# Optimization experiments

Hardware: AMD Instinct MI355X
Metric: run time of the kernel (lower is better)

## Reference

```python
import jax, jax.numpy as jnp
import numpy as np

B, N = 128, 196
ENC, DEC, ATT = 2048, 512, 512

def setup_inputs() -> dict:
    key = jax.random.key(0)
    ks = jax.random.split(key, 8)
    s_enc = 1.0 / np.sqrt(ENC)
    s_dec = 1.0 / np.sqrt(DEC)
    s_att = 1.0 / np.sqrt(ATT)
    return {
        "encoder_out": jax.random.normal(ks[0], (B, N, ENC), jnp.float32),
        "decoder_hidden": jax.random.normal(ks[1], (B, DEC), jnp.float32),
        "W_enc": jax.random.uniform(ks[2], (ENC, ATT), jnp.float32, -s_enc, s_enc),
        "b_enc": jax.random.uniform(ks[3], (ATT,), jnp.float32, -s_enc, s_enc),
        "W_dec": jax.random.uniform(ks[4], (DEC, ATT), jnp.float32, -s_dec, s_dec),
        "b_dec": jax.random.uniform(ks[5], (ATT,), jnp.float32, -s_dec, s_dec),
        "W_full": jax.random.uniform(ks[6], (ATT,), jnp.float32, -s_att, s_att),
        "b_full": jax.random.uniform(ks[7], (), jnp.float32, -s_att, s_att),
    }

def reference(encoder_out, decoder_hidden, W_enc, b_enc, W_dec, b_dec, W_full, b_full):
    # att1: [B, N, ATT]; att2: [B, 1, ATT]
    att1 = jnp.einsum('bne,ea->bna', encoder_out, W_enc) + b_enc
    att2 = decoder_hidden @ W_dec + b_dec
    combined = jax.nn.relu(att1 + att2[:, None, :])
    e = jnp.einsum('bna,a->bn', combined, W_full) + b_full  # [B, N]
    alpha = jax.nn.softmax(e, axis=1)
    attention_weighted_encoding = jnp.einsum('bne,bn->be', encoder_out, alpha)
    return attention_weighted_encoding, alpha
```

## Files before the change

kernel.cpp:

```cpp
#include <hip/hip_runtime.h>
#include <hip/hip_bf16.h>

#define BB   128
#define NN   196
#define MM   (BB*NN)
#define ENC  2048
#define ATT  512
#define DEC  512
#define BK   32
#define KSTEPS (ENC/BK)

using f32x4 = __attribute__((ext_vector_type(4))) float;
using s16x8 = __attribute__((ext_vector_type(8))) short;

__device__ __forceinline__ short f2bf(float f) {
    union { __hip_bfloat16 h; short s; } u;
    u.h = __float2bfloat16(f);
    return u.s;
}

__global__ void transpose_convert_kernel(const float* __restrict__ W,
                                         unsigned short* __restrict__ Wt) {
    __shared__ float tile[32][33];
    const int a0 = blockIdx.x * 32;
    const int k0 = blockIdx.y * 32;
    const int tx = threadIdx.x & 31, ty = threadIdx.x >> 5;
    #pragma unroll
    for (int i = 0; i < 32; i += 8)
        tile[ty + i][tx] = W[(size_t)(k0 + ty + i) * ATT + a0 + tx];
    __syncthreads();
    #pragma unroll
    for (int i = 0; i < 32; i += 8) {
        union { __hip_bfloat16 h; unsigned short u; } v;
        v.h = __float2bfloat16(tile[tx][ty + i]);
        Wt[(size_t)(a0 + ty + i) * ENC + k0 + tx] = v.u;
    }
}

__global__ void att2_kernel(const float* __restrict__ dec,
                            const float* __restrict__ Wd,
                            const float* __restrict__ bd,
                            const float* __restrict__ benc,
                            float* __restrict__ att2) {
    const int b  = blockIdx.x;
    const int c0 = blockIdx.y * 64;
    const int t  = threadIdx.x;
    const int cl = t & 63, kg = t >> 6;
    __shared__ float sdec[DEC];
    __shared__ float red[4][64];
    sdec[t]       = dec[b * DEC + t];
    sdec[t + 256] = dec[b * DEC + t + 256];
    __syncthreads();
    float acc = 0.f;
    const float* wp = Wd + c0 + cl;
    #pragma unroll 8
    for (int k = kg * 128; k < kg * 128 + 128; ++k)
        acc += sdec[k] * wp[(size_t)k * ATT];
    red[kg][cl] = acc;
    __syncthreads();
    if (t < 64) {
        float s = red[0][t] + red[1][t] + red[2][t] + red[3][t];
        att2[b * ATT + c0 + t] = s + bd[c0 + t] + benc[c0 + t];
    }
}

__global__ __launch_bounds__(256, 5)
void gemm_e_kernel(const float* __restrict__ enc,
                   const unsigned short* __restrict__ Wt,
                   const float* __restrict__ att2,
                   const float* __restrict__ Wf,
                   float* __restrict__ e_part) {
    __shared__ float sA[64 * 32];
    __shared__ unsigned short sB[128 * 32];
    __shared__ float e_sm[64];

    const int t    = threadIdx.x;
    const int lane = t & 63;
    const int w    = t >> 6;
    const int aBlk  = blockIdx.x;
    const int mBase = blockIdx.y * 64;
    const int aBase = aBlk * 128;
    const int r = lane & 15, q = lane >> 4;

    const float* gA[2];
    #pragma unroll
    for (int i = 0; i < 2; ++i) {
        int s = i * 256 + t;
        int row = s >> 3, ck = s & 7;
        int g = ck ^ (row & 7);
        gA[i] = enc + (size_t)(mBase + row) * ENC + g * 4;
    }
    const unsigned short* gB[2];
    #pragma unroll
    for (int i = 0; i < 2; ++i) {
        int s = i * 256 + t;
        int row = s >> 2, ck = s & 3;
        int g = ck ^ ((row & 3) ^ ((row >> 2) & 3));
        gB[i] = Wt + (size_t)(aBase + row) * ENC + g * 8;
    }

    int offA[4][2];
    #pragma unroll
    for (int mi = 0; mi < 4; ++mi) {
        int row = mi * 16 + r;
        offA[mi][0] = row * 128 + ((2 * q)     ^ (row & 7)) * 16;
        offA[mi][1] = row * 128 + ((2 * q + 1) ^ (row & 7)) * 16;
    }
    int offB[2];
    #pragma unroll
    for (int ni = 0; ni < 2; ++ni) {
        int col = w * 32 + ni * 16 + r;
        offB[ni] = col * 64 + (q ^ ((col & 3) ^ ((col >> 2) & 3))) * 16;
    }

    f32x4 acc[4][2] = {};

    #pragma unroll 1
    for (int ks = 0; ks < KSTEPS; ++ks) {
        #pragma unroll
        for (int i = 0; i < 2; ++i)
            __builtin_amdgcn_global_load_lds(
                (const __attribute__((address_space(1))) void*)(gA[i] + (size_t)ks * BK),
                (__attribute__((address_space(3))) void*)((char*)sA + (i * 256 + w * 64) * 16),
                16, 0, 0);
        #pragma unroll
        for (int i = 0; i < 2; ++i)
            __builtin_amdgcn_global_load_lds(
                (const __attribute__((address_space(1))) void*)(gB[i] + (size_t)ks * BK),
                (__attribute__((address_space(3))) void*)((char*)sB + (i * 256 + w * 64) * 16),
                16, 0, 0);
        __syncthreads();

        s16x8 af[4], bf[2];
        #pragma unroll
        for (int mi = 0; mi < 4; ++mi) {
            f32x4 f0 = *(const f32x4*)((const char*)sA + offA[mi][0]);
            f32x4 f1 = *(const f32x4*)((const char*)sA + offA[mi][1]);
            s16x8 a;
            #pragma unroll
            for (int j = 0; j < 4; ++j) { a[j] = f2bf(f0[j]); a[4 + j] = f2bf(f1[j]); }
            af[mi] = a;
        }
        #pragma unroll
        for (int ni = 0; ni < 2; ++ni)
            bf[ni] = *(const s16x8*)((const char*)sB + offB[ni]);

        #pragma unroll
        for (int mi = 0; mi < 4; ++mi)
            #pragma unroll
            for (int ni = 0; ni < 2; ++ni)
                acc[mi][ni] = __builtin_amdgcn_mfma_f32_16x16x32_bf16(
                    af[mi], bf[ni], acc[mi][ni], 0, 0, 0);
        __syncthreads();
    }

    if (t < 64) e_sm[t] = 0.f;
    __syncthreads();

    float wfv[2];
    #pragma unroll
    for (int ni = 0; ni < 2; ++ni)
        wfv[ni] = Wf[aBase + w * 32 + ni * 16 + r];

    #pragma unroll
    for (int mi = 0; mi < 4; ++mi) {
        #pragma unroll
        for (int reg = 0; reg < 4; ++reg) {
            int lrow = mi * 16 + q * 4 + reg;
            int gm = mBase + lrow;
            int b = gm / NN;
            const float* a2 = att2 + b * ATT + aBase + w * 32;
            float rs = 0.f;
            #pragma unroll
            for (int ni = 0; ni < 2; ++ni) {
                float v = acc[mi][ni][reg] + a2[ni * 16 + r];
                rs += fmaxf(v, 0.f) * wfv[ni];
            }
            rs += __shfl_xor(rs, 1);
            rs += __shfl_xor(rs, 2);
            rs += __shfl_xor(rs, 4);
            rs += __shfl_xor(rs, 8);
            if (r == 0) atomicAdd(&e_sm[lrow], rs);
        }
    }
    __syncthreads();
    if (t < 64)
        e_part[(size_t)aBlk * MM + mBase + t] = e_sm[t];
}

__global__ void softmax_kernel(const float* __restrict__ e_part,
                               const float* __restrict__ b_full,
                               float* __restrict__ out,
                               float* __restrict__ alpha_ws) {
    const int b = blockIdx.x;
    const int t = threadIdx.x;
    __shared__ float sm[256];

    float v = -3.0e38f;
    if (t < NN) {
        int gm = b * NN + t;
        v = e_part[gm] + e_part[MM + gm] + e_part[2 * MM + gm] + e_part[3 * MM + gm]
            + b_full[0];
    }
    sm[t] = v;
    __syncthreads();
    for (int s = 128; s > 0; s >>= 1) {
        if (t < s) sm[t] = fmaxf(sm[t], sm[t + s]);
        __syncthreads();
    }
    float mx = sm[0];
    __syncthreads();
    float ex = (t < NN) ? __expf(v - mx) : 0.f;
    sm[t] = ex;
    __syncthreads();
    for (int s = 128; s > 0; s >>= 1) {
        if (t < s) sm[t] += sm[t + s];
        __syncthreads();
    }
    float inv = 1.0f / sm[0];
    if (t < NN) {
        float a = ex * inv;
        out[BB * ENC + b * NN + t] = a;
        alpha_ws[b * NN + t] = a;
    }
}

__global__ __launch_bounds__(256)
void awe_kernel(const float* __restrict__ enc,
                const float* __restrict__ alpha_ws,
                float* __restrict__ out) {
    const int b = blockIdx.x, chunk = blockIdx.y;
    const int t = threadIdx.x;
    __shared__ float al[NN];
    if (t < NN) al[t] = alpha_ws[b * NN + t];
    __syncthreads();

    const float* ep = enc + (size_t)b * NN * ENC + chunk * 1024 + t * 4;
    f32x4 acc0 = {}, acc1 = {}, acc2 = {}, acc3 = {};
    #pragma unroll 2
    for (int n = 0; n < NN; n += 4) {
        f32x4 v0 = *(const f32x4*)(ep + (size_t)(n + 0) * ENC);
        f32x4 v1 = *(const f32x4*)(ep + (size_t)(n + 1) * ENC);
        f32x4 v2 = *(const f32x4*)(ep + (size_t)(n + 2) * ENC);
        f32x4 v3 = *(const f32x4*)(ep + (size_t)(n + 3) * ENC);
        acc0 += v0 * al[n];
        acc1 += v1 * al[n + 1];
        acc2 += v2 * al[n + 2];
        acc3 += v3 * al[n + 3];
    }
    f32x4 s = (acc0 + acc1) + (acc2 + acc3);
    *(f32x4*)(out + (size_t)b * ENC + chunk * 1024 + t * 4) = s;
}

extern "C" void kernel_launch(void* const* d_in, const int* in_sizes, int n_in,
                              void* d_out, int out_size, void* d_ws, size_t ws_size,
                              hipStream_t stream) {
    const float* enc    = (const float*)d_in[0];
    const float* dec    = (const float*)d_in[1];
    const float* W_enc  = (const float*)d_in[2];
    const float* b_enc  = (const float*)d_in[3];
    const float* W_dec  = (const float*)d_in[4];
    const float* b_dec  = (const float*)d_in[5];
    const float* W_full = (const float*)d_in[6];
    const float* b_full = (const float*)d_in[7];
    float* out = (float*)d_out;

    char* ws = (char*)d_ws;
    unsigned short* Wt = (unsigned short*)ws;
    float* att2     = (float*)(ws + (size_t)ENC * ATT * 2);
    float* e_part   = (float*)(ws + (size_t)ENC * ATT * 2 + BB * ATT * 4);
    float* alpha_ws = (float*)(ws + (size_t)ENC * ATT * 2 + BB * ATT * 4
                               + (size_t)4 * MM * 4);

    transpose_convert_kernel<<<dim3(ATT / 32, ENC / 32), 256, 0, stream>>>(W_enc, Wt);
    att2_kernel<<<dim3(BB, 8), 256, 0, stream>>>(dec, W_dec, b_dec, b_enc, att2);
    gemm_e_kernel<<<dim3(4, MM / 64), 256, 0, stream>>>(enc, Wt, att2, W_full, e_part);
    softmax_kernel<<<BB, 256, 0, stream>>>(e_part, b_full, out, alpha_ws);
    awe_kernel<<<dim3(BB, 2), 256, 0, stream>>>(enc, alpha_ws, out);
}
```

Baseline: 457.2 us.

## Pre-convert encoder_out to bf16 and use DMA-to-LDS bf16 GEMM path

Adds a pass that converts encoder_out to bf16 in workspace. The GEMM then loads both operands as bf16 via global_load_lds with a wider 256-column tile, producing 2 partial sums instead of 4. The weighted-sum kernel also reads the bf16 copy. This halves the bytes read by the two later passes, at the cost of an extra full read and write of encoder_out. It also lowers precision in the final weighted sum, and the path only runs when the workspace is large enough.

```diff
diff --git a/kernel.cpp b/kernel.cpp
--- a/kernel.cpp
+++ b/kernel.cpp
@@ -12,11 +12,18 @@
 
 using f32x4 = __attribute__((ext_vector_type(4))) float;
 using s16x8 = __attribute__((ext_vector_type(8))) short;
+using u16x4 = __attribute__((ext_vector_type(4))) unsigned short;
+using u16x8 = __attribute__((ext_vector_type(8))) unsigned short;
 
 __device__ __forceinline__ short f2bf(float f) {
     union { __hip_bfloat16 h; short s; } u;
     u.h = __float2bfloat16(f);
     return u.s;
+}
+__device__ __forceinline__ float bf2f(unsigned short u) {
+    union { unsigned int i; float f; } v;
+    v.i = ((unsigned int)u) << 16;
+    return v.f;
 }
 
 __global__ void transpose_convert_kernel(const float* __restrict__ W,
@@ -35,6 +42,23 @@
         v.h = __float2bfloat16(tile[tx][ty + i]);
         Wt[(size_t)(a0 + ty + i) * ENC + k0 + tx] = v.u;
     }
+}
+
+__global__ __launch_bounds__(256)
+void enc_cvt_kernel(const float* __restrict__ enc,
+                    unsigned short* __restrict__ encb) {
+    const size_t row = blockIdx.x;
+    const int t = threadIdx.x;
+    const float* in = enc + row * ENC + t * 8;
+    f32x4 a = *(const f32x4*)in;
+    f32x4 b = *(const f32x4*)(in + 4);
+    u16x8 o;
+    #pragma unroll
+    for (int j = 0; j < 4; ++j) {
+        o[j]     = (unsigned short)f2bf(a[j]);
+        o[4 + j] = (unsigned short)f2bf(b[j]);
+    }
+    *(u16x8*)(encb + row * ENC + t * 8) = o;
 }
 
 __global__ void att2_kernel(const float* __restrict__ dec,
@@ -62,6 +86,108 @@
         float s = red[0][t] + red[1][t] + red[2][t] + red[3][t];
         att2[b * ATT + c0 + t] = s + bd[c0 + t] + benc[c0 + t];
     }
+}
+
+__global__ __launch_bounds__(256, 4)
+void gemm_bf16_kernel(const unsigned short* __restrict__ encb,
+                      const unsigned short* __restrict__ Wt,
+                      const float* __restrict__ att2,
+                      const float* __restrict__ Wf,
+                      float* __restrict__ e_part) {
+    __shared__ unsigned short sA[64 * 32];
+    __shared__ unsigned short sB[256 * 32];
+    __shared__ float e_sm[64];
+
+    const int t    = threadIdx.x;
+    const int lane = t & 63;
+    const int w    = t >> 6;
+    const int aBlk  = blockIdx.x;
+    const int mBase = blockIdx.y * 64;
+    const int aBase = aBlk * 256;
+    const int r = lane & 15, q = lane >> 4;
+
+    const unsigned short* gA = encb + (size_t)(mBase + (t >> 2)) * ENC + (t & 3) * 8;
+    const unsigned short* gB[4];
+    #pragma unroll
+    for (int i = 0; i < 4; ++i) {
+        int s = i * 256 + t;
+        gB[i] = Wt + (size_t)(aBase + (s >> 2)) * ENC + (s & 3) * 8;
+    }
+
+    int offA[4];
+    #pragma unroll
+    for (int mi = 0; mi < 4; ++mi)
+        offA[mi] = (mi * 16 + r) * 64 + q * 16;
+    int offB[4];
+    #pragma unroll
+    for (int ni = 0; ni < 4; ++ni)
+        offB[ni] = (w * 64 + ni * 16 + r) * 64 + q * 16;
+
+    f32x4 acc[4][4] = {};
+
+    #pragma unroll 1
+    for (int ks = 0; ks < KSTEPS; ++ks) {
+        __builtin_amdgcn_global_load_lds(
+            (const __attribute__((address_space(1))) void*)(gA + (size_t)ks * BK),
+            (__attribute__((address_space(3))) void*)((char*)sA + t * 16),
+            16, 0, 0);
+        #pragma unroll
+        for (int i = 0; i < 4; ++i)
+            __builtin_amdgcn_global_load_lds(
+                (const __attribute__((address_space(1))) void*)(gB[i] + (size_t)ks * BK),
+                (__attribute__((address_space(3))) void*)((char*)sB + (i * 256 + t) * 16),
+                16, 0, 0);
+        __syncthreads();
+
+        s16x8 af[4], bf[4];
+        #pragma unroll
+        for (int mi = 0; mi < 4; ++mi)
+            af[mi] = *(const s16x8*)((const char*)sA + offA[mi]);
+        #pragma unroll
+        for (int ni = 0; ni < 4; ++ni)
+            bf[ni] = *(const s16x8*)((const char*)sB + offB[ni]);
+
+        #pragma unroll
+        for (int mi = 0; mi < 4; ++mi)
+            #pragma unroll
+            for (int ni = 0; ni < 4; ++ni)
+                acc[mi][ni] = __builtin_amdgcn_mfma_f32_16x16x32_bf16(
+                    af[mi], bf[ni], acc[mi][ni], 0, 0, 0);
+        __syncthreads();
+    }
+
+    if (t < 64) e_sm[t] = 0.f;
+    __syncthreads();
+
+    float wfv[4];
+    #pragma unroll
+    for (int ni = 0; ni < 4; ++ni)
+        wfv[ni] = Wf[aBase + w * 64 + ni * 16 + r];
+
+    #pragma unroll
+    for (int mi = 0; mi < 4; ++mi) {
+        #pragma unroll
+        for (int reg = 0; reg < 4; ++reg) {
+            int lrow = mi * 16 + q * 4 + reg;
+            int gm = mBase + lrow;
+            int b = gm / NN;
+            const float* a2 = att2 + b * ATT + aBase + w * 64;
+            float rs = 0.f;
+            #pragma unroll
+            for (int ni = 0; ni < 4; ++ni) {
+                float v = acc[mi][ni][reg] + a2[ni * 16 + r];
+                rs += fmaxf(v, 0.f) * wfv[ni];
+            }
+            rs += __shfl_xor(rs, 1);
+            rs += __shfl_xor(rs, 2);
+            rs += __shfl_xor(rs, 4);
+            rs += __shfl_xor(rs, 8);
+            if (r == 0) atomicAdd(&e_sm[lrow], rs);
+        }
+    }
+    __syncthreads();
+    if (t < 64)
+        e_part[(size_t)aBlk * MM + mBase + t] = e_sm[t];
 }
 
 __global__ __launch_bounds__(256, 5)
@@ -191,7 +317,8 @@
 __global__ void softmax_kernel(const float* __restrict__ e_part,
                                const float* __restrict__ b_full,
                                float* __restrict__ out,
-                               float* __restrict__ alpha_ws) {
+                               float* __restrict__ alpha_ws,
+                               int nparts) {
     const int b = blockIdx.x;
     const int t = threadIdx.x;
     __shared__ float sm[256];
@@ -199,8 +326,9 @@
     float v = -3.0e38f;
     if (t < NN) {
         int gm = b * NN + t;
-        v = e_part[gm] + e_part[MM + gm] + e_part[2 * MM + gm] + e_part[3 * MM + gm]
-            + b_full[0];
+        float s = b_full[0];
+        for (int p = 0; p < nparts; ++p) s += e_part[(size_t)p * MM + gm];
+        v = s;
     }
     sm[t] = v;
     __syncthreads();
@@ -223,6 +351,36 @@
         out[BB * ENC + b * NN + t] = a;
         alpha_ws[b * NN + t] = a;
     }
+}
+
+__global__ __launch_bounds__(256)
+void awe_bf16_kernel(const unsigned short* __restrict__ encb,
+                     const float* __restrict__ alpha_ws,
+                     float* __restrict__ out) {
+    const int b = blockIdx.x, chunk = blockIdx.y;
+    const int t = threadIdx.x;
+    __shared__ float al[NN];
+    if (t < NN) al[t] = alpha_ws[b * NN + t];
+    __syncthreads();
+
+    const unsigned short* ep = encb + (size_t)b * NN * ENC + chunk * 1024 + t * 4;
+    f32x4 acc0 = {}, acc1 = {}, acc2 = {}, acc3 = {};
+    #pragma unroll 2
+    for (int n = 0; n < NN; n += 4) {
+        u16x4 v0 = *(const u16x4*)(ep + (size_t)(n + 0) * ENC);
+        u16x4 v1 = *(const u16x4*)(ep + (size_t)(n + 1) * ENC);
+        u16x4 v2 = *(const u16x4*)(ep + (size_t)(n + 2) * ENC);
+        u16x4 v3 = *(const u16x4*)(ep + (size_t)(n + 3) * ENC);
+        #pragma unroll
+        for (int j = 0; j < 4; ++j) {
+            acc0[j] += bf2f(v0[j]) * al[n];
+            acc1[j] += bf2f(v1[j]) * al[n + 1];
+            acc2[j] += bf2f(v2[j]) * al[n + 2];
+            acc3[j] += bf2f(v3[j]) * al[n + 3];
+        }
+    }
+    f32x4 s = (acc0 + acc1) + (acc2 + acc3);
+    *(f32x4*)(out + (size_t)b * ENC + chunk * 1024 + t * 4) = s;
 }
 
 __global__ __launch_bounds__(256)
@@ -267,14 +425,23 @@
 
     char* ws = (char*)d_ws;
     unsigned short* Wt = (unsigned short*)ws;
-    float* att2     = (float*)(ws + (size_t)ENC * ATT * 2);
-    float* e_part   = (float*)(ws + (size_t)ENC * ATT * 2 + BB * ATT * 4);
-    float* alpha_ws = (float*)(ws + (size_t)ENC * ATT * 2 + BB * ATT * 4
-                               + (size_t)4 * MM * 4);
+    float* att2     = (float*)(ws + 2097152);
+    float* e_part   = (float*)(ws + 2359296);
+    float* alpha_ws = (float*)(ws + 2760704);
+    unsigned short* encb = (unsigned short*)(ws + 3145728);
+    const size_t WS_NEED = 3145728 + (size_t)MM * ENC * 2;
 
     transpose_convert_kernel<<<dim3(ATT / 32, ENC / 32), 256, 0, stream>>>(W_enc, Wt);
     att2_kernel<<<dim3(BB, 8), 256, 0, stream>>>(dec, W_dec, b_dec, b_enc, att2);
-    gemm_e_kernel<<<dim3(4, MM / 64), 256, 0, stream>>>(enc, Wt, att2, W_full, e_part);
-    softmax_kernel<<<BB, 256, 0, stream>>>(e_part, b_full, out, alpha_ws);
-    awe_kernel<<<dim3(BB, 2), 256, 0, stream>>>(enc, alpha_ws, out);
-}
+
+    if (ws_size >= WS_NEED) {
+        enc_cvt_kernel<<<MM, 256, 0, stream>>>(enc, encb);
+        gemm_bf16_kernel<<<dim3(2, MM / 64), 256, 0, stream>>>(encb, Wt, att2, W_full, e_part);
+        softmax_kernel<<<BB, 256, 0, stream>>>(e_part, b_full, out, alpha_ws, 2);
+        awe_bf16_kernel<<<dim3(BB, 2), 256, 0, stream>>>(encb, alpha_ws, out);
+    } else {
+        gemm_e_kernel<<<dim3(4, MM / 64), 256, 0, stream>>>(enc, Wt, att2, W_full, e_part);
+        softmax_kernel<<<BB, 256, 0, stream>>>(e_part, b_full, out, alpha_ws, 4);
+        awe_kernel<<<dim3(BB, 2), 256, 0, stream>>>(enc, alpha_ws, out);
+    }
+}
```

New measurement: 445.8 us. 2.5% less time.
